# Kernel optimization log

Measured on AMD Instinct MI355X. Metric: run time of the kernel, lower is better.

Reference implementation:

```python
import jax, jax.numpy as jnp
import numpy as np

N_NODES = 50000
N_EDGES = 800000
IN_DIM = 128
HID_DIM = 128
NUM_GRAPHS = 64


def gcn_conv(x, edge_index, W, b):
    """PyG GCNConv: symmetric-normalized aggregation with self-loops.
    out = D^{-1/2} (A + I) D^{-1/2} (x @ W) + b
    """
    n = x.shape[0]
    loop = jnp.arange(n, dtype=edge_index.dtype)
    src = jnp.concatenate([edge_index[0], loop])  # [E+N]
    dst = jnp.concatenate([edge_index[1], loop])
    deg = jax.ops.segment_sum(jnp.ones_like(dst, x.dtype), dst, num_segments=n)
    dinv = jnp.where(deg > 0, jax.lax.rsqrt(deg), 0.0)
    norm = dinv[src] * dinv[dst]  # [E+N]
    h = x @ W  # [N, H] transform before propagate (PyG order)
    msg = h[src] * norm[:, None]  # [E+N, H] gathered+scaled messages
    out = jax.ops.segment_sum(msg, dst, num_segments=n)  # scatter-add
    return out + b


def global_mean_pool(x, batch, num_graphs):
    s = jax.ops.segment_sum(x, batch, num_segments=num_graphs)
    cnt = jax.ops.segment_sum(jnp.ones((x.shape[0],), x.dtype), batch, num_segments=num_graphs)
    return s / jnp.maximum(cnt, 1.0)[:, None]


def setup_inputs() -> dict:
    key = jax.random.key(0)
    ks = jax.random.split(key, 8)
    x = jax.random.normal(ks[0], (N_NODES, IN_DIM), dtype=jnp.float32)
    edge_index = jax.random.randint(ks[1], (2, N_EDGES), 0, N_NODES, dtype=jnp.int64)
    batch = jnp.sort(jax.random.randint(ks[2], (N_NODES,), 0, NUM_GRAPHS, dtype=jnp.int64))
    s1 = 1.0 / np.sqrt(IN_DIM)
    s2 = 1.0 / np.sqrt(HID_DIM)
    W1 = jax.random.uniform(ks[3], (IN_DIM, HID_DIM), jnp.float32, -s1, s1)
    b1 = jnp.zeros((HID_DIM,), jnp.float32)
    W2 = jax.random.uniform(ks[4], (HID_DIM, HID_DIM), jnp.float32, -s2, s2)
    b2 = jnp.zeros((HID_DIM,), jnp.float32)
    Wc = jax.random.uniform(ks[5], (HID_DIM, 1), jnp.float32, -s2, s2)
    bc = jnp.zeros((1,), jnp.float32)
    return {"x": x, "edge_index": edge_index, "batch": batch,
            "W1": W1, "b1": b1, "W2": W2, "b2": b2, "Wc": Wc, "bc": bc}


def reference(x, edge_index, batch, W1, b1, W2, b2, Wc, bc):
    h = jax.nn.relu(gcn_conv(x, edge_index, W1, b1))
    # dropout p=0.1 is identity in eval mode
    h = gcn_conv(h, edge_index, W2, b2)
    g = global_mean_pool(h, batch, NUM_GRAPHS)  # [G, H]
    return jax.nn.sigmoid(g @ Wc + bc)  # [G, 1]
```

## Files before the change

kernel.cpp:

```cpp
#include <hip/hip_runtime.h>
#include <hip/hip_bf16.h>
#include <hip/hip_fp16.h>

#define N_NODES 50000
#define N_EDGES 800000
#define DIM     128
#define NG      64
#define GN      16
#define CAP     48
#define AGG_EB  256
#define LAXP    136

#define BUILD_B 782
#define CAST_B  1563
#define VB_B    129
#define WF_B    8

typedef float  f2_t  __attribute__((ext_vector_type(2)));
typedef float  f32x4 __attribute__((ext_vector_type(4)));
typedef _Float16 f16x8 __attribute__((ext_vector_type(8)));
typedef _Float16 f16x4 __attribute__((ext_vector_type(4)));

__global__ void k_prep(const int* __restrict__ ei, int* __restrict__ deg,
                       unsigned short* __restrict__ csr,
                       const float* __restrict__ W2, const float* __restrict__ Wc,
                       const float* __restrict__ b2, float* __restrict__ v,
                       float* __restrict__ beta2,
                       const float* __restrict__ W1, f16x8* __restrict__ w1f) {
    __shared__ float red[4];
    int bid = blockIdx.x, t = threadIdx.x;
    if (bid < BUILD_B) {
        int base = bid * 1024;
        #pragma unroll
        for (int k = 0; k < 4; k++) {
            int e = base + k * 256 + t;
            if (e < N_EDGES) {
                int s = ei[e];
                int d = ei[N_EDGES + e];
                int pos = atomicAdd(&deg[d], 1);
                if (pos < CAP) csr[(size_t)d * CAP + pos] = (unsigned short)s;
            }
        }
    } else if (bid < BUILD_B + VB_B) {
        int b = bid - BUILD_B;
        float p = 0.f;
        if (t < DIM) p = (b < DIM) ? W2[b * DIM + t] * Wc[t] : b2[t] * Wc[t];
        #pragma unroll
        for (int off = 32; off > 0; off >>= 1) p += __shfl_down(p, off, 64);
        if ((t & 63) == 0) red[t >> 6] = p;
        __syncthreads();
        if (t == 0) {
            float s = red[0] + red[1];
            if (b < DIM) v[b] = s; else beta2[0] = s;
        }
    } else {
        int idx = (bid - (BUILD_B + VB_B)) * 256 + t;
        int ntile = idx >> 8, kb = (idx >> 6) & 3, l = idx & 63;
        int kbase = kb * 32 + (l >> 4) * 8;
        int n = ntile * 16 + (l & 15);
        f16x8 o;
        #pragma unroll
        for (int j = 0; j < 8; j++) o[j] = (_Float16)W1[(kbase + j) * DIM + n];
        w1f[idx] = o;
    }
}

__global__ void k_cast(const float4* __restrict__ x4, uint4* __restrict__ xq4,
                       const int* __restrict__ deg, const int* __restrict__ batch,
                       unsigned int* __restrict__ bd) {
    int idx = blockIdx.x * 256 + threadIdx.x;
    if (idx >= (N_NODES + 1) * 8) return;
    if (idx >= N_NODES * 8) {
        xq4[idx] = make_uint4(0u, 0u, 0u, 0u);
        return;
    }
    int node = idx >> 3;
    float di = rsqrtf((float)deg[node] + 1.f);
    uint4 o;
    unsigned* op = (unsigned*)&o;
    #pragma unroll
    for (int q = 0; q < 4; q++) {
        float4 f = x4[idx * 4 + q];
        int p = 0;
        p = __builtin_amdgcn_cvt_pk_fp8_f32(di * f.x, di * f.y, p, false);
        p = __builtin_amdgcn_cvt_pk_fp8_f32(di * f.z, di * f.w, p, true);
        op[q] = (unsigned)p;
    }
    xq4[idx] = o;
    if ((idx & 7) == 0) {
        unsigned hw = (unsigned)__half_as_ushort(__float2half(di));
        bd[node] = ((unsigned)batch[node] & 0xFFFFu) | (hw << 16);
    }
}

__global__ __launch_bounds__(512) void k_node(
    const unsigned int* __restrict__ xq,
    const unsigned short* __restrict__ csr,
    const f16x8* __restrict__ w1f,
    const float* __restrict__ b1,
    const float* __restrict__ v, const int* __restrict__ deg,
    float* __restrict__ z2) {
    __shared__ _Float16 laxh[GN * LAXP];
    __shared__ float redm[GN * 8];
    int tid = threadIdx.x;
    int w = tid >> 6, l = tid & 63;
    int half = l >> 5, hl = l & 31;
    int node0 = blockIdx.x * GN;

    {
        int i = node0 + 2 * w + half;
        int dg = deg[i];
        int len = min(dg, CAP);
        float di = rsqrtf((float)dg + 1.f);

        unsigned su = xq[(size_t)i * 32 + hl];
        f2_t s01 = __builtin_amdgcn_cvt_pk_f32_fp8((int)su, false);
        f2_t s23 = __builtin_amdgcn_cvt_pk_f32_fp8((int)su, true);
        float ax[8], ay[8], az[8], aw[8];
        #pragma unroll
        for (int k = 0; k < 8; k++) { ax[k] = 0.f; ay[k] = 0.f; az[k] = 0.f; aw[k] = 0.f; }
        ax[0] = s01.x; ay[0] = s01.y;
        az[0] = s23.x; aw[0] = s23.y;

        int lenmax = max(len, __shfl_xor(len, 32, 64));
        int lmp = (lenmax + 7) & ~7;
        const uint4* csr4 = (const uint4*)(csr + (size_t)i * CAP);
        for (int j = 0; j < lmp; j += 8) {
            uint4 cw = csr4[j >> 3];
            unsigned cw8[4] = {cw.x, cw.y, cw.z, cw.w};
            unsigned q[8];
            #pragma unroll
            for (int k = 0; k < 8; k++) {
                unsigned id = (cw8[k >> 1] >> ((k & 1) * 16)) & 0xFFFFu;
                unsigned idc = (j + k < len) ? id : (unsigned)N_NODES;
                q[k] = xq[(size_t)idc * 32 + hl];
            }
            #pragma unroll
            for (int k = 0; k < 8; k++) {
                f2_t e01 = __builtin_amdgcn_cvt_pk_f32_fp8((int)q[k], false);
                f2_t e23 = __builtin_amdgcn_cvt_pk_f32_fp8((int)q[k], true);
                ax[k] += e01.x; ay[k] += e01.y;
                az[k] += e23.x; aw[k] += e23.y;
            }
        }
        float a0 = 0.f, a1 = 0.f, a2 = 0.f, a3 = 0.f;
        #pragma unroll
        for (int k = 0; k < 8; k++) { a0 += ax[k]; a1 += ay[k]; a2 += az[k]; a3 += aw[k]; }
        f16x4 pk;
        pk[0] = (_Float16)(di * a0); pk[1] = (_Float16)(di * a1);
        pk[2] = (_Float16)(di * a2); pk[3] = (_Float16)(di * a3);
        *(f16x4*)&laxh[(2 * w + half) * LAXP + 4 * hl] = pk;
    }
    __syncthreads();

    f32x4 acc = {0.f, 0.f, 0.f, 0.f};
    #pragma unroll
    for (int kb = 0; kb < 4; kb++) {
        f16x8 af = *(const f16x8*)&laxh[(l & 15) * LAXP + kb * 32 + (l >> 4) * 8];
        f16x8 bf = w1f[(w * 4 + kb) * 64 + l];
        acc = __builtin_amdgcn_mfma_f32_16x16x32_f16(af, bf, acc, 0, 0, 0);
    }
    int n = w * 16 + (l & 15);
    float bn = b1[n], vn = v[n];
    #pragma unroll
    for (int r = 0; r < 4; r++) {
        float p = fmaxf(acc[r] + bn, 0.f) * vn;
        p += __shfl_xor(p, 1, 64);
        p += __shfl_xor(p, 2, 64);
        p += __shfl_xor(p, 4, 64);
        p += __shfl_xor(p, 8, 64);
        if ((l & 15) == 0) redm[((l >> 4) * 4 + r) * 8 + w] = p;
    }
    __syncthreads();
    if (tid < GN) {
        float s = 0.f;
        #pragma unroll
        for (int q = 0; q < 8; q++) s += redm[tid * 8 + q];
        z2[node0 + tid] = rsqrtf((float)deg[node0 + tid] + 1.f) * s;
    }
}

__global__ void k_aggz(const float* __restrict__ z2, const unsigned int* __restrict__ bd,
                       const int* __restrict__ ei, const int* __restrict__ batch,
                       float* __restrict__ gpartE, float* __restrict__ gpartN,
                       int* __restrict__ gcnt) {
    int bid = blockIdx.x, t = threadIdx.x;
    if (bid < AGG_EB) {
        __shared__ float bs[4][NG];
        bs[t >> 6][t & 63] = 0.f;
        __syncthreads();
        int wg = t >> 6;
        for (int base = bid * 1024; base < N_EDGES; base += AGG_EB * 1024) {
            #pragma unroll
            for (int k = 0; k < 4; k++) {
                int e = base + k * 256 + t;
                if (e < N_EDGES) {
                    int s = ei[e];
                    int d = ei[N_EDGES + e];
                    unsigned u = bd[d];
                    float dv = __half2float(__ushort_as_half((unsigned short)(u >> 16)));
                    atomicAdd(&bs[wg][u & 63u], dv * z2[s]);
                }
            }
        }
        __syncthreads();
        if (t < NG) gpartE[bid * NG + t] = bs[0][t] + bs[1][t] + bs[2][t] + bs[3][t];
    } else {
        __shared__ int range[2];
        __shared__ float rs[4];
        int g = bid - AGG_EB;
        if (t < 2) {
            int key = g + t;
            int lo = 0, hi = N_NODES;
            while (lo < hi) { int m = (lo + hi) >> 1; if (batch[m] < key) lo = m + 1; else hi = m; }
            range[t] = lo;
        }
        __syncthreads();
        int lo = range[0], hi = range[1];
        float loc = 0.f;
        for (int i = lo + t; i < hi; i += 256)
            loc += __half2float(__ushort_as_half((unsigned short)(bd[i] >> 16))) * z2[i];
        #pragma unroll
        for (int off = 32; off > 0; off >>= 1) loc += __shfl_down(loc, off, 64);
        if ((t & 63) == 0) rs[t >> 6] = loc;
        __syncthreads();
        if (t == 0) {
            gpartN[g] = rs[0] + rs[1] + rs[2] + rs[3];
            gcnt[g] = hi - lo;
        }
    }
}

__global__ void k_final(const float* __restrict__ gpartE, const float* __restrict__ gpartN,
                        const int* __restrict__ gcnt, const float* __restrict__ beta2,
                        const float* __restrict__ bcin, float* __restrict__ out) {
    __shared__ float acc[4][NG];
    int t = threadIdx.x;
    int g = t & 63, c = t >> 6;
    float s = 0.f;
    for (int k = 0; k < AGG_EB / 4; k++)
        s += gpartE[(c * (AGG_EB / 4) + k) * NG + g];
    acc[c][g] = s;
    __syncthreads();
    if (t < NG) {
        float tot = acc[0][t] + acc[1][t] + acc[2][t] + acc[3][t] + gpartN[t];
        int cnt = gcnt[t];
        float val = tot / (float)(cnt > 0 ? cnt : 1) + beta2[0] + bcin[0];
        out[t] = 1.f / (1.f + expf(-val));
    }
}

extern "C" void kernel_launch(void* const* d_in, const int* in_sizes, int n_in,
                              void* d_out, int out_size, void* d_ws, size_t ws_size,
                              hipStream_t stream) {
    const float* x   = (const float*)d_in[0];
    const int*   ei  = (const int*)  d_in[1];
    const int*   bat = (const int*)  d_in[2];
    const float* W1  = (const float*)d_in[3];
    const float* b1  = (const float*)d_in[4];
    const float* W2  = (const float*)d_in[5];
    const float* b2  = (const float*)d_in[6];
    const float* Wc  = (const float*)d_in[7];
    const float* bc  = (const float*)d_in[8];
    float* out = (float*)d_out;

    char* w = (char*)d_ws;
    size_t off = 0;
    auto alloc = [&](size_t bytes) -> void* {
        void* p = w + off;
        off = (off + bytes + 255) & ~(size_t)255;
        return p;
    };
    int*   deg     = (int*)  alloc(N_NODES * 4);
    size_t zero_len = off;
    float* z2      = (float*)alloc(N_NODES * 4);
    float* v       = (float*)alloc(DIM * 4);
    float* beta2   = (float*)alloc(4);
    float* gpartE  = (float*)alloc((size_t)AGG_EB * NG * 4);
    float* gpartN  = (float*)alloc(NG * 4);
    int*   gcnt    = (int*)  alloc(NG * 4);
    unsigned int* bd = (unsigned int*)alloc(N_NODES * 4);
    f16x8* w1f     = (f16x8*)alloc(2048 * 16);
    unsigned int* xq = (unsigned int*)alloc((size_t)(N_NODES + 1) * DIM);
    unsigned short* csr = (unsigned short*)alloc((size_t)N_NODES * CAP * 2);
    (void)ws_size; (void)in_sizes; (void)n_in; (void)out_size;

    hipMemsetAsync(d_ws, 0, zero_len, stream);

    dim3 b256(256);
    k_prep<<<dim3(BUILD_B + VB_B + WF_B), b256, 0, stream>>>(
        ei, deg, csr, W2, Wc, b2, v, beta2, W1, w1f);
    k_cast<<<dim3(CAST_B), b256, 0, stream>>>(
        (const float4*)x, (uint4*)xq, deg, bat, bd);
    k_node<<<dim3(N_NODES / GN), dim3(512), 0, stream>>>(
        xq, csr, w1f, b1, v, deg, z2);
    k_aggz<<<dim3(AGG_EB + NG), b256, 0, stream>>>(z2, bd, ei, bat, gpartE, gpartN, gcnt);
    k_final<<<dim3(1), b256, 0, stream>>>(gpartE, gpartN, gcnt, beta2, bc, out);
}
```

Before: 193.3 us.

## Build CSR via two-pass bucketed counting sort by destination bin

Replaces the direct global-atomic CSR build, where each edge does an atomicAdd on deg[dst] and a scattered 2-byte store, with a counting sort over 256-node destination bins. A histogram pass feeds a scatter pass that writes packed (src, dst_low) words into bin-contiguous order. A per-bin kernel then builds the CSR rows using shared-memory atomics. This aims to remove contended global atomics and random writes, at the cost of two extra kernel launches, re-reading the edge list, and an extra 3.2 MB intermediate buffer.

New measurement: 165.9 us. -14.2%, faster.

```diff
diff --git a/kernel.cpp b/kernel.cpp
--- a/kernel.cpp
+++ b/kernel.cpp
@@ -11,7 +11,10 @@
 #define AGG_EB  256
 #define LAXP    136
 
-#define BUILD_B 782
+#define NBIN    196
+#define SORT_B  250
+#define EPB     3200
+
 #define CAST_B  1563
 #define VB_B    129
 #define WF_B    8
@@ -21,28 +24,29 @@
 typedef _Float16 f16x8 __attribute__((ext_vector_type(8)));
 typedef _Float16 f16x4 __attribute__((ext_vector_type(4)));
 
-__global__ void k_prep(const int* __restrict__ ei, int* __restrict__ deg,
-                       unsigned short* __restrict__ csr,
+__global__ void k_prep(const int* __restrict__ ei, int* __restrict__ binCnt,
                        const float* __restrict__ W2, const float* __restrict__ Wc,
                        const float* __restrict__ b2, float* __restrict__ v,
                        float* __restrict__ beta2,
                        const float* __restrict__ W1, f16x8* __restrict__ w1f) {
     __shared__ float red[4];
+    __shared__ int hist[256];
     int bid = blockIdx.x, t = threadIdx.x;
-    if (bid < BUILD_B) {
-        int base = bid * 1024;
-        #pragma unroll
-        for (int k = 0; k < 4; k++) {
-            int e = base + k * 256 + t;
-            if (e < N_EDGES) {
-                int s = ei[e];
-                int d = ei[N_EDGES + e];
-                int pos = atomicAdd(&deg[d], 1);
-                if (pos < CAP) csr[(size_t)d * CAP + pos] = (unsigned short)s;
+    if (bid < SORT_B) {
+        hist[t] = 0;
+        __syncthreads();
+        int base = bid * EPB;
+        for (int r = 0; r < 13; r++) {
+            int idx = r * 256 + t;
+            if (idx < EPB) {
+                int d = ei[N_EDGES + base + idx];
+                atomicAdd(&hist[d >> 8], 1);
             }
         }
-    } else if (bid < BUILD_B + VB_B) {
-        int b = bid - BUILD_B;
+        __syncthreads();
+        if (t < NBIN && hist[t] > 0) atomicAdd(&binCnt[t], hist[t]);
+    } else if (bid < SORT_B + VB_B) {
+        int b = bid - SORT_B;
         float p = 0.f;
         if (t < DIM) p = (b < DIM) ? W2[b * DIM + t] * Wc[t] : b2[t] * Wc[t];
         #pragma unroll
@@ -54,7 +58,7 @@
             if (b < DIM) v[b] = s; else beta2[0] = s;
         }
     } else {
-        int idx = (bid - (BUILD_B + VB_B)) * 256 + t;
+        int idx = (bid - (SORT_B + VB_B)) * 256 + t;
         int ntile = idx >> 8, kb = (idx >> 6) & 3, l = idx & 63;
         int kbase = kb * 32 + (l >> 4) * 8;
         int n = ntile * 16 + (l & 15);
@@ -63,6 +67,71 @@
         for (int j = 0; j < 8; j++) o[j] = (_Float16)W1[(kbase + j) * DIM + n];
         w1f[idx] = o;
     }
+}
+
+__global__ void k_scatter(const int* __restrict__ ei, const int* __restrict__ binCnt,
+                          int* __restrict__ binCur, int* __restrict__ binOff,
+                          unsigned int* __restrict__ sorted) {
+    __shared__ int soff[256];
+    __shared__ int hist[256];
+    __shared__ int cur[256];
+    int bid = blockIdx.x, t = threadIdx.x;
+    int c = (t < NBIN) ? binCnt[t] : 0;
+    soff[t] = c;
+    #pragma unroll
+    for (int o = 1; o < 256; o <<= 1) {
+        __syncthreads();
+        int v2 = (t >= o) ? soff[t - o] : 0;
+        __syncthreads();
+        soff[t] += v2;
+    }
+    __syncthreads();
+    int excl = soff[t] - c;
+    if (bid == 0 && t < NBIN) binOff[t] = excl;
+    hist[t] = 0;
+    __syncthreads();
+    int base = bid * EPB;
+    for (int r = 0; r < 13; r++) {
+        int idx = r * 256 + t;
+        if (idx < EPB) {
+            int d = ei[N_EDGES + base + idx];
+            atomicAdd(&hist[d >> 8], 1);
+        }
+    }
+    __syncthreads();
+    if (t < NBIN && hist[t] > 0) cur[t] = excl + atomicAdd(&binCur[t], hist[t]);
+    __syncthreads();
+    for (int r = 0; r < 13; r++) {
+        int idx = r * 256 + t;
+        if (idx < EPB) {
+            int e = base + idx;
+            int s = ei[e];
+            int d = ei[N_EDGES + e];
+            int pos = atomicAdd(&cur[d >> 8], 1);
+            sorted[pos] = (unsigned)s | ((unsigned)(d & 255) << 16);
+        }
+    }
+}
+
+__global__ __launch_bounds__(512) void k_csr(const unsigned int* __restrict__ sorted,
+                      const int* __restrict__ binOff, int* __restrict__ deg,
+                      unsigned short* __restrict__ csr) {
+    __shared__ int cur[256];
+    int b = blockIdx.x, t = threadIdx.x;
+    if (t < 256) cur[t] = 0;
+    __syncthreads();
+    int lo = binOff[b];
+    int hi = (b == NBIN - 1) ? N_EDGES : binOff[b + 1];
+    for (int i = lo + t; i < hi; i += 512) {
+        unsigned e = sorted[i];
+        unsigned src = e & 0xFFFFu;
+        unsigned dLow = e >> 16;
+        int pos = atomicAdd(&cur[dLow], 1);
+        if (pos < CAP) csr[(size_t)(b * 256 + dLow) * CAP + pos] = (unsigned short)src;
+    }
+    __syncthreads();
+    int node = b * 256 + t;
+    if (t < 256 && node < N_NODES) deg[node] = cur[t];
 }
 
 __global__ void k_cast(const float4* __restrict__ x4, uint4* __restrict__ xq4,
@@ -271,8 +340,11 @@
         off = (off + bytes + 255) & ~(size_t)255;
         return p;
     };
+    int*   binCnt  = (int*)  alloc(NBIN * 4);
+    int*   binCur  = (int*)  alloc(NBIN * 4);
+    size_t zero_len = off;
+    int*   binOff  = (int*)  alloc(NBIN * 4);
     int*   deg     = (int*)  alloc(N_NODES * 4);
-    size_t zero_len = off;
     float* z2      = (float*)alloc(N_NODES * 4);
     float* v       = (float*)alloc(DIM * 4);
     float* beta2   = (float*)alloc(4);
@@ -282,14 +354,17 @@
     unsigned int* bd = (unsigned int*)alloc(N_NODES * 4);
     f16x8* w1f     = (f16x8*)alloc(2048 * 16);
     unsigned int* xq = (unsigned int*)alloc((size_t)(N_NODES + 1) * DIM);
+    unsigned int* sorted = (unsigned int*)alloc((size_t)N_EDGES * 4);
     unsigned short* csr = (unsigned short*)alloc((size_t)N_NODES * CAP * 2);
     (void)ws_size; (void)in_sizes; (void)n_in; (void)out_size;
 
     hipMemsetAsync(d_ws, 0, zero_len, stream);
 
     dim3 b256(256);
-    k_prep<<<dim3(BUILD_B + VB_B + WF_B), b256, 0, stream>>>(
-        ei, deg, csr, W2, Wc, b2, v, beta2, W1, w1f);
+    k_prep<<<dim3(SORT_B + VB_B + WF_B), b256, 0, stream>>>(
+        ei, binCnt, W2, Wc, b2, v, beta2, W1, w1f);
+    k_scatter<<<dim3(SORT_B), b256, 0, stream>>>(ei, binCnt, binCur, binOff, sorted);
+    k_csr<<<dim3(NBIN), dim3(512), 0, stream>>>(sorted, binOff, deg, csr);
     k_cast<<<dim3(CAST_B), b256, 0, stream>>>(
         (const float4*)x, (uint4*)xq, deg, bat, bd);
     k_node<<<dim3(N_NODES / GN), dim3(512), 0, stream>>>(
```
